# Kernel tuning notes

Measured on AMD Instinct MI355X. Metric: run time of the kernel, lower is better.

Reference implementation:

```python
import jax, jax.numpy as jnp
import numpy as np

DIM = 192
HEADS = 6
HEAD_DIM = DIM // HEADS
SCALE = HEAD_DIM ** -0.5
WIN = (2, 6, 12)  # (pl, lat, lon)
RES = (8, 96, 360)
TOW = (RES[0] // WIN[0]) * (RES[1] // WIN[1])  # type_of_windows = 64
N = WIN[0] * WIN[1] * WIN[2]  # 144
NW = TOW
B_ = 1 * (RES[2] // WIN[2])  # 30
TABLE = WIN[0] ** 2 * WIN[1] ** 2 * (2 * WIN[2] - 1)  # 3312


def get_earth_position_index(ws):
    wpl, wlat, wlon = ws
    czi = np.arange(wpl)
    czj = -np.arange(wpl) * wpl
    chi = np.arange(wlat)
    chj = -np.arange(wlat) * wlat
    cw = np.arange(wlon)
    c1 = np.stack(np.meshgrid(czi, chi, cw, indexing='ij'))
    c2 = np.stack(np.meshgrid(czj, chj, cw, indexing='ij'))
    f1 = c1.reshape(3, -1)
    f2 = c2.reshape(3, -1)
    coords = (f1[:, :, None] - f2[:, None, :]).transpose(1, 2, 0).copy()
    coords[:, :, 2] += wlon - 1
    coords[:, :, 1] *= 2 * wlon - 1
    coords[:, :, 0] *= (2 * wlon - 1) * wlat * wlat
    return coords.sum(-1)  # [N, N]


def setup_inputs() -> dict:
    key = jax.random.key(0)
    ks = jax.random.split(key, 6)
    x = jax.random.normal(ks[0], (B_, NW, N, DIM), dtype=jnp.float32)
    qkv_w = jax.random.normal(ks[1], (3 * DIM, DIM), dtype=jnp.float32) * 0.02
    qkv_b = jnp.zeros((3 * DIM,), dtype=jnp.float32)
    proj_w = jax.random.normal(ks[2], (DIM, DIM), dtype=jnp.float32) * 0.02
    proj_b = jnp.zeros((DIM,), dtype=jnp.float32)
    bias_table = jax.random.normal(ks[3], (TABLE, TOW, HEADS), dtype=jnp.float32) * 0.02
    pos_index = jnp.asarray(get_earth_position_index(WIN), dtype=jnp.int32)
    return {"x": x, "qkv_w": qkv_w, "qkv_b": qkv_b, "proj_w": proj_w,
            "proj_b": proj_b, "bias_table": bias_table, "pos_index": pos_index}


def reference(x, qkv_w, qkv_b, proj_w, proj_b, bias_table, pos_index):
    Bw, nW, n, C = x.shape
    # fused qkv projection
    qkv = jnp.einsum('bwnc,dc->bwnd', x, qkv_w) + qkv_b
    qkv = qkv.reshape(Bw, nW, n, 3, HEADS, HEAD_DIM)
    q = qkv[..., 0, :, :].transpose(0, 3, 1, 2, 4) * SCALE  # [B,H,W,N,hd]
    k = qkv[..., 1, :, :].transpose(0, 3, 1, 2, 4)
    v = qkv[..., 2, :, :].transpose(0, 3, 1, 2, 4)
    attn = jnp.einsum('bhwnd,bhwmd->bhwnm', q, k)  # [B,H,W,N,N]
    # gathered earth position bias: [N,N,TOW,H] -> [H,TOW,N,N]
    bias = bias_table[pos_index.reshape(-1)].reshape(n, n, TOW, HEADS)
    bias = bias.transpose(3, 2, 0, 1)
    attn = attn + bias[None]
    attn = jax.nn.softmax(attn, axis=-1)
    out = jnp.einsum('bhwnm,bhwmd->bhwnd', attn, v)
    out = out.transpose(0, 2, 3, 1, 4).reshape(Bw, nW, n, C)
    out = jnp.einsum('bwnc,dc->bwnd', out, proj_w) + proj_b
    return out
```

## Files before the change

kernel.cpp:

```cpp
#include <hip/hip_runtime.h>

typedef unsigned short u16;
typedef unsigned int u32;

#define NTOK 144
#define CDIM 192
#define NHEADS 6
#define HDIM 32
#define NWIN 64
#define NB 30
#define NBLK (NB * NWIN)
#define TABLE_N 3312
#define SCALE 0.17677669529663687f

typedef __bf16 bf16x8 __attribute__((ext_vector_type(8)));
typedef u16 u16x8 __attribute__((ext_vector_type(8)));
typedef u16 u16x4 __attribute__((ext_vector_type(4)));
typedef float f32x4 __attribute__((ext_vector_type(4)));

__device__ __forceinline__ float bf2f(u16 u) {
    union { u32 i; float f; } v; v.i = ((u32)u) << 16; return v.f;
}
__device__ __forceinline__ u16 f2bf(float f) {
    union { float f; u32 i; } v; v.f = f;
    u32 r = v.i + 0x7FFFu + ((v.i >> 16) & 1u);
    return (u16)(r >> 16);
}

__device__ __forceinline__ bf16x8 ld_frag(const void* base, size_t idx, int fm) {
    if (!fm) return *(const bf16x8*)((const u16*)base + idx);
    const float* pf = (const float*)base;
    u16x8 t;
#pragma unroll
    for (int j = 0; j < 8; ++j) t[j] = f2bf(pf[idx + j]);
    union { u16x8 u; bf16x8 b; } cv; cv.u = t; return cv.b;
}
__device__ __forceinline__ float ld_s(const void* base, size_t idx, int fm) {
    return fm ? ((const float*)base)[idx] : bf2f(((const u16*)base)[idx]);
}
__device__ __forceinline__ void st_s(void* base, size_t idx, float v, int fm) {
    if (fm) ((float*)base)[idx] = v; else ((u16*)base)[idx] = f2bf(v);
}
__device__ __forceinline__ bf16x8 zero_frag() {
    union { u16x8 u; bf16x8 b; } cv;
#pragma unroll
    for (int j = 0; j < 8; ++j) cv.u[j] = 0;
    return cv.b;
}
__device__ __forceinline__ bf16x8 ld_x_frag(const void* x, size_t rowbase, int off, int fm) {
    if (!fm) return *(const bf16x8*)((const u16*)x + rowbase + off);
    const float* xs = (const float*)x + rowbase + off;
    const float4 a0 = *(const float4*)xs;
    const float4 a1 = *(const float4*)(xs + 4);
    union { u16x8 u; bf16x8 b; } cv;
    cv.u[0] = f2bf(a0.x); cv.u[1] = f2bf(a0.y); cv.u[2] = f2bf(a0.z); cv.u[3] = f2bf(a0.w);
    cv.u[4] = f2bf(a1.x); cv.u[5] = f2bf(a1.y); cv.u[6] = f2bf(a1.z); cv.u[7] = f2bf(a1.w);
    return cv.b;
}

__global__ void detect_mode(const u16* __restrict__ w, int* __restrict__ flag) {
    __shared__ int cnt;
    if (threadIdx.x == 0) cnt = 0;
    __syncthreads();
    int h = 0;
    for (int i = threadIdx.x; i < 4096; i += 256) {
        int e = (w[i] >> 7) & 0xFF;
        if (e >= 0x8E) h++;
    }
    atomicAdd(&cnt, h);
    __syncthreads();
    if (threadIdx.x == 0) flag[0] = (cnt > 64) ? 1 : 0;
}

__global__ void bias_gather3(const void* __restrict__ table, const int* __restrict__ pos,
                             u16* __restrict__ bias_f, const int* __restrict__ mode) {
    __shared__ u16 smT[TABLE_N];
    const int fm = mode[0];
    const int w = blockIdx.x / NHEADS, h = blockIdx.x % NHEADS;
    for (int t = threadIdx.x; t < TABLE_N; t += 256) {
        size_t j = (size_t)t * (NWIN * NHEADS) + w * NHEADS + h;
        smT[t] = fm ? f2bf(((const float*)table)[j]) : ((const u16*)table)[j];
    }
    __syncthreads();
    u16* o = bias_f + (size_t)(w * NHEADS + h) * (81 * 256);
    for (int i = threadIdx.x; i < 81 * 256; i += 256) {
        int T = i / 2304, rem2 = i % 2304;
        int nt = rem2 >> 8, lane = (rem2 >> 2) & 63, r = rem2 & 3;
        int row = T * 16 + (lane >> 4) * 4 + r;
        int col = nt * 16 + (lane & 15);
        o[i] = smT[pos[row * NTOK + col]];
    }
}

__global__ void wconv(const void* __restrict__ qkv_w, const void* __restrict__ qkv_b,
                      const void* __restrict__ proj_w, const void* __restrict__ proj_b,
                      u16* __restrict__ qkvw_c, u16* __restrict__ projw_c,
                      u16* __restrict__ qkvb_c, u16* __restrict__ projb_c,
                      const int* __restrict__ mode) {
    const int fm = mode[0];
    const int gid = blockIdx.x * blockDim.x + threadIdx.x;
    const int np  = gridDim.x * blockDim.x;
    const int NQW = 3 * CDIM * CDIM, NPW = CDIM * CDIM;
    if (fm) {
        const float* a = (const float*)qkv_w;
        const float* b = (const float*)proj_w;
        const float* c = (const float*)qkv_b;
        const float* d = (const float*)proj_b;
        for (int i = gid; i < NQW; i += np) qkvw_c[i] = f2bf(a[i]);
        for (int i = gid; i < NPW; i += np) projw_c[i] = f2bf(b[i]);
        for (int i = gid; i < 3 * CDIM; i += np) qkvb_c[i] = f2bf(c[i]);
        for (int i = gid; i < CDIM; i += np) projb_c[i] = f2bf(d[i]);
    } else {
        const u16* a = (const u16*)qkv_w;
        const u16* b = (const u16*)proj_w;
        const u16* c = (const u16*)qkv_b;
        const u16* d = (const u16*)proj_b;
        for (int i = gid; i < NQW; i += np) qkvw_c[i] = a[i];
        for (int i = gid; i < NPW; i += np) projw_c[i] = b[i];
        for (int i = gid; i < 3 * CDIM; i += np) qkvb_c[i] = c[i];
        for (int i = gid; i < CDIM; i += np) projb_c[i] = d[i];
    }
}

#define AQ_OFF  0
#define AK_OFF  5760
#define AQK_STR 40
#define APB_OFF 11520
#define AP_STR  152
#define AW_STR  200
#define AVT_OFF 33408
#define AVT_STR 152
#define ASM_TOT 38272

__global__ __launch_bounds__(576, 8)
void attn_qkv(const void* __restrict__ x,
              const u16* __restrict__ qkvw_c, const u16* __restrict__ qkvb_c,
              const u16* __restrict__ bias_f, u16* __restrict__ o_ws,
              const int* __restrict__ mode) {
    __shared__ __align__(16) u16 sm[ASM_TOT];

    const int fm   = mode[0];
    const int tid  = threadIdx.x;
    const int wv   = tid >> 6;
    const int lane = tid & 63;
    const int l15  = lane & 15;
    const int lq   = lane >> 4;

    const int blk   = blockIdx.x;
    const int virt  = (blk & 7) * (NBLK / 8) + (blk >> 3);
    const int w     = virt / NB;
    const int bwlin = (virt % NB) * NWIN + w;

    const size_t xrow = ((size_t)bwlin * NTOK + wv * 16 + l15) * CDIM;
    const f32x4 fzero = {0.f, 0.f, 0.f, 0.f};

    for (int h = 0; h < NHEADS; ++h) {
        const int hoff = h * HDIM;

        for (int i = tid; i < 96 * CDIM / 8; i += 576) {
            int r = i / 24, c8 = (i % 24) * 8;
            int grow = (r >> 5) * CDIM + hoff + (r & 31);
            *(uint4*)&sm[APB_OFF + r * AW_STR + c8] =
                *(const uint4*)(qkvw_c + (size_t)grow * CDIM + c8);
        }
        __syncthreads();

        {
            f32x4 acc[6];
#pragma unroll
            for (int nt = 0; nt < 6; ++nt) acc[nt] = fzero;
#pragma unroll
            for (int kt = 0; kt < 6; ++kt) {
                bf16x8 xf = ld_x_frag(x, xrow, kt * 32 + lq * 8, fm);
#pragma unroll
                for (int nt = 0; nt < 6; ++nt) {
                    bf16x8 bb = *(const bf16x8*)&sm[APB_OFF + (nt * 16 + l15) * AW_STR + kt * 32 + lq * 8];
                    acc[nt] = __builtin_amdgcn_mfma_f32_16x16x32_bf16(xf, bb, acc[nt], 0, 0, 0);
                }
            }
#pragma unroll
            for (int nt = 0; nt < 6; ++nt) {
                int col = nt * 16 + l15;
                int s = col >> 5, d = col & 31;
                float bias = bf2f(qkvb_c[s * CDIM + hoff + d]);
#pragma unroll
                for (int r = 0; r < 4; ++r) {
                    int row = wv * 16 + lq * 4 + r;
                    float v = acc[nt][r] + bias;
                    if (s == 0)      sm[AQ_OFF + row * AQK_STR + d] = f2bf(v * SCALE);
                    else if (s == 1) sm[AK_OFF + row * AQK_STR + d] = f2bf(v);
                    else             sm[AVT_OFF + d * AVT_STR + row] = f2bf(v);
                }
            }
        }
        __syncthreads();

        f32x4 sacc[9];
        {
            bf16x8 a = *(const bf16x8*)&sm[AQ_OFF + (wv * 16 + l15) * AQK_STR + lq * 8];
#pragma unroll
            for (int nt = 0; nt < 9; ++nt) {
                bf16x8 bb = *(const bf16x8*)&sm[AK_OFF + (nt * 16 + l15) * AQK_STR + lq * 8];
                sacc[nt] = __builtin_amdgcn_mfma_f32_16x16x32_bf16(a, bb, fzero, 0, 0, 0);
            }
            const u16* bf = bias_f + ((size_t)(w * NHEADS + h) * 81 + wv * 9) * 256;
#pragma unroll
            for (int nt = 0; nt < 9; ++nt) {
                u16x4 pk = *(const u16x4*)&bf[nt * 256 + (lane << 2)];
#pragma unroll
                for (int r = 0; r < 4; ++r) sacc[nt][r] += bf2f(pk[r]);
            }
#pragma unroll
            for (int r = 0; r < 4; ++r) {
                float m = -1e30f;
                for (int nt = 0; nt < 9; ++nt) m = fmaxf(m, sacc[nt][r]);
                for (int d = 1; d < 16; d <<= 1) m = fmaxf(m, __shfl_xor(m, d, 64));
                float s = 0.f;
                for (int nt = 0; nt < 9; ++nt) {
                    float e = __expf(sacc[nt][r] - m);
                    sacc[nt][r] = e; s += e;
                }
                for (int d = 1; d < 16; d <<= 1) s += __shfl_xor(s, d, 64);
                float inv = 1.0f / s;
                for (int nt = 0; nt < 9; ++nt) sacc[nt][r] *= inv;
            }
        }

#pragma unroll
        for (int r = 0; r < 4; ++r) {
            int row = wv * 16 + lq * 4 + r;
#pragma unroll
            for (int nt = 0; nt < 9; ++nt)
                sm[APB_OFF + row * AP_STR + nt * 16 + l15] = f2bf(sacc[nt][r]);
        }
        __syncthreads();

        {
            f32x4 pv[2] = {fzero, fzero};
#pragma unroll
            for (int kt = 0; kt < 4; ++kt) {
                bf16x8 a = *(const bf16x8*)&sm[APB_OFF + (wv * 16 + l15) * AP_STR + kt * 32 + lq * 8];
#pragma unroll
                for (int dt = 0; dt < 2; ++dt) {
                    bf16x8 bb = *(const bf16x8*)&sm[AVT_OFF + (dt * 16 + l15) * AVT_STR + kt * 32 + lq * 8];
                    pv[dt] = __builtin_amdgcn_mfma_f32_16x16x32_bf16(a, bb, pv[dt], 0, 0, 0);
                }
            }
            bf16x8 a4 = zero_frag();
            if (lq < 2)
                a4 = *(const bf16x8*)&sm[APB_OFF + (wv * 16 + l15) * AP_STR + 128 + lq * 8];
#pragma unroll
            for (int dt = 0; dt < 2; ++dt) {
                bf16x8 bb = *(const bf16x8*)&sm[AVT_OFF + (dt * 16 + l15) * AVT_STR + 128 + (lq & 1) * 8];
                pv[dt] = __builtin_amdgcn_mfma_f32_16x16x32_bf16(a4, bb, pv[dt], 0, 0, 0);
            }
            u16* op = o_ws + (((size_t)h * NBLK + bwlin) * NTOK + wv * 16 + lq * 4) * HDIM;
#pragma unroll
            for (int dt = 0; dt < 2; ++dt)
#pragma unroll
                for (int r = 0; r < 4; ++r)
                    op[r * HDIM + dt * 16 + l15] = f2bf(pv[dt][r]);
        }
        __syncthreads();
    }
}

#define PW_STR 200
__global__ __launch_bounds__(512, 4)
void proj_gemm(const u16* __restrict__ o_ws, const u16* __restrict__ projw_c,
               const u16* __restrict__ projb_c, void* __restrict__ out,
               const int* __restrict__ mode) {
    __shared__ __align__(16) u16 smW[CDIM * PW_STR];
    const int fm   = mode[0];
    const int tid  = threadIdx.x;
    const int wv   = tid >> 6;
    const int lane = tid & 63;
    const int l15  = lane & 15;
    const int lq   = lane >> 4;

    for (int i = tid; i < CDIM * CDIM / 8; i += 512) {
        int r = i / 24, c8 = (i % 24) * 8;
        *(uint4*)&smW[r * PW_STR + c8] = *(const uint4*)(projw_c + (size_t)r * CDIM + c8);
    }
    __syncthreads();

    const int tile = blockIdx.x * 8 + wv;
    const int win  = tile / 9;
    const int trow = (tile % 9) * 16;
    const f32x4 fzero = {0.f, 0.f, 0.f, 0.f};

    bf16x8 a[6];
#pragma unroll
    for (int kt = 0; kt < 6; ++kt)
        a[kt] = *(const bf16x8*)&o_ws[((size_t)kt * NBLK + win) * (NTOK * HDIM)
                                      + (trow + l15) * HDIM + lq * 8];

    f32x4 acc[12];
#pragma unroll
    for (int nt = 0; nt < 12; ++nt) acc[nt] = fzero;
#pragma unroll
    for (int kt = 0; kt < 6; ++kt) {
#pragma unroll
        for (int nt = 0; nt < 12; ++nt) {
            bf16x8 bb = *(const bf16x8*)&smW[(nt * 16 + l15) * PW_STR + kt * 32 + lq * 8];
            acc[nt] = __builtin_amdgcn_mfma_f32_16x16x32_bf16(a[kt], bb, acc[nt], 0, 0, 0);
        }
    }
    const size_t rb = (size_t)win * (NTOK * CDIM) + (size_t)trow * CDIM;
#pragma unroll
    for (int nt = 0; nt < 12; ++nt) {
        int col = nt * 16 + l15;
        float pb = bf2f(projb_c[col]);
#pragma unroll
        for (int r = 0; r < 4; ++r)
            st_s(out, rb + (lq * 4 + r) * CDIM + col, acc[nt][r] + pb, fm);
    }
}

#define Q_OFF  0
#define K_OFF  5760
#define QK_STR 40
#define P_OFF  11520
#define P_STR  168
#define VT_OFF 35712
#define VT_STR 168
#define OA_OFF 41088
#define OA_STR 200
#define SM_TOT 69888

template<int FASTW>
__global__ __launch_bounds__(576, 3)
void earth_attn_fused(const void* __restrict__ x, const void* __restrict__ qkv_w,
                const void* __restrict__ qkv_b, const void* __restrict__ proj_w,
                const void* __restrict__ proj_b, const void* __restrict__ bias_table,
                const int* __restrict__ pos_index,
                const u16* __restrict__ qkvw_c, const u16* __restrict__ projw_c,
                const u16* __restrict__ qkvb_c, const u16* __restrict__ projb_c,
                const u16* __restrict__ bias_f, int use_bias_f,
                void* __restrict__ out, const int* __restrict__ mode) {
    __shared__ __align__(16) u16 sm[SM_TOT];

    const int fm   = mode[0];
    const int tid  = threadIdx.x;
    const int wv   = tid >> 6;
    const int lane = tid & 63;
    const int l15  = lane & 15;
    const int lq   = lane >> 4;

    const int blk   = blockIdx.x;
    const int virt  = (blk & 7) * (NBLK / 8) + (blk >> 3);
    const int w     = virt / NB;
    const int bwlin = (virt % NB) * NWIN + w;

    {
        uint4 z; z.x = z.y = z.z = z.w = 0u;
        for (int i = tid; i < (32 * VT_STR) / 8; i += 576) *(uint4*)&sm[VT_OFF + i * 8] = z;
    }

    bf16x8 xfrag[6];
    {
        const size_t xrow = ((size_t)bwlin * NTOK + wv * 16 + l15) * CDIM;
#pragma unroll
        for (int kt = 0; kt < 6; ++kt) xfrag[kt] = ld_x_frag(x, xrow, kt * 32 + lq * 8, fm);
    }
    __syncthreads();

    const f32x4 fzero = {0.f, 0.f, 0.f, 0.f};

    for (int h = 0; h < NHEADS; ++h) {
        const int hoff = h * HDIM;

        float bsv[9][4];
        if (FASTW || use_bias_f) {
            const u16* bf = bias_f + ((size_t)(w * NHEADS + h) * 81 + wv * 9) * 256;
#pragma unroll
            for (int nt = 0; nt < 9; ++nt) {
                u16x4 pk = *(const u16x4*)&bf[nt * 256 + (lane << 2)];
#pragma unroll
                for (int r = 0; r < 4; ++r) bsv[nt][r] = bf2f(pk[r]);
            }
        } else {
#pragma unroll
            for (int nt = 0; nt < 9; ++nt) {
                int col = nt * 16 + l15;
#pragma unroll
                for (int r = 0; r < 4; ++r) {
                    int idx = pos_index[(wv * 16 + lq * 4 + r) * NTOK + col];
                    bsv[nt][r] = ld_s(bias_table, ((size_t)idx * NWIN + w) * NHEADS + h, fm);
                }
            }
        }

        {
            f32x4 acc[6];
            for (int nt = 0; nt < 6; ++nt) acc[nt] = fzero;
            int wrow[6];
#pragma unroll
            for (int nt = 0; nt < 6; ++nt) {
                int c = nt * 16 + l15, s = c >> 5, d = c & 31;
                wrow[nt] = (s * CDIM + hoff + d) * CDIM;
            }
#pragma unroll
            for (int kt = 0; kt < 6; ++kt) {
#pragma unroll
                for (int nt = 0; nt < 6; ++nt) {
                    bf16x8 bb = FASTW
                        ? *(const bf16x8*)&qkvw_c[(size_t)wrow[nt] + kt * 32 + lq * 8]
                        : ld_frag(qkv_w, (size_t)wrow[nt] + kt * 32 + lq * 8, fm);
                    acc[nt] = __builtin_amdgcn_mfma_f32_16x16x32_bf16(xfrag[kt], bb, acc[nt], 0, 0, 0);
                }
            }
#pragma unroll
            for (int nt = 0; nt < 6; ++nt) {
                int col = nt * 16 + l15;
                int s = col >> 5, d = col & 31;
                float bias = FASTW ? bf2f(qkvb_c[s * CDIM + hoff + d])
                                   : ld_s(qkv_b, s * CDIM + hoff + d, fm);
#pragma unroll
                for (int r = 0; r < 4; ++r) {
                    int row = wv * 16 + lq * 4 + r;
                    float v = acc[nt][r] + bias;
                    if (s == 0)      sm[Q_OFF + row * QK_STR + d] = f2bf(v * SCALE);
                    else if (s == 1) sm[K_OFF + row * QK_STR + d] = f2bf(v);
                    else             sm[VT_OFF + d * VT_STR + row] = f2bf(v);
                }
            }
        }
        __syncthreads();

        f32x4 sacc[9];
        {
            bf16x8 a = *(const bf16x8*)&sm[Q_OFF + (wv * 16 + l15) * QK_STR + lq * 8];
#pragma unroll
            for (int nt = 0; nt < 9; ++nt) {
                bf16x8 bb = *(const bf16x8*)&sm[K_OFF + (nt * 16 + l15) * QK_STR + lq * 8];
                sacc[nt] = __builtin_amdgcn_mfma_f32_16x16x32_bf16(a, bb, fzero, 0, 0, 0);
            }
#pragma unroll
            for (int nt = 0; nt < 9; ++nt)
#pragma unroll
                for (int r = 0; r < 4; ++r) sacc[nt][r] += bsv[nt][r];
#pragma unroll
            for (int r = 0; r < 4; ++r) {
                float m = -1e30f;
                for (int nt = 0; nt < 9; ++nt) m = fmaxf(m, sacc[nt][r]);
                for (int d = 1; d < 16; d <<= 1) m = fmaxf(m, __shfl_xor(m, d, 64));
                float s = 0.f;
                for (int nt = 0; nt < 9; ++nt) {
                    float e = __expf(sacc[nt][r] - m);
                    sacc[nt][r] = e; s += e;
                }
                for (int d = 1; d < 16; d <<= 1) s += __shfl_xor(s, d, 64);
                float inv = 1.0f / s;
                for (int nt = 0; nt < 9; ++nt) sacc[nt][r] *= inv;
            }
        }

#pragma unroll
        for (int r = 0; r < 4; ++r) {
            int row = wv * 16 + lq * 4 + r;
#pragma unroll
            for (int nt = 0; nt < 9; ++nt)
                sm[P_OFF + row * P_STR + nt * 16 + l15] = f2bf(sacc[nt][r]);
            sm[P_OFF + row * P_STR + 144 + l15] = 0;
        }
        __syncthreads();

        f32x4 pv[2] = {fzero, fzero};
#pragma unroll
        for (int kt = 0; kt < 5; ++kt) {
            bf16x8 a = *(const bf16x8*)&sm[P_OFF + (wv * 16 + l15) * P_STR + kt * 32 + lq * 8];
#pragma unroll
            for (int dt = 0; dt < 2; ++dt) {
                bf16x8 bb = *(const bf16x8*)&sm[VT_OFF + (dt * 16 + l15) * VT_STR + kt * 32 + lq * 8];
                pv[dt] = __builtin_amdgcn_mfma_f32_16x16x32_bf16(a, bb, pv[dt], 0, 0, 0);
            }
        }

#pragma unroll
        for (int dt = 0; dt < 2; ++dt)
#pragma unroll
            for (int r = 0; r < 4; ++r) {
                int row = wv * 16 + lq * 4 + r;
                sm[OA_OFF + row * OA_STR + hoff + dt * 16 + l15] = f2bf(pv[dt][r]);
            }
        __syncthreads();
    }

    f32x4 oacc[12];
    for (int nt = 0; nt < 12; ++nt) oacc[nt] = fzero;
    {
        bf16x8 a[6];
#pragma unroll
        for (int kt = 0; kt < 6; ++kt)
            a[kt] = *(const bf16x8*)&sm[OA_OFF + (wv * 16 + l15) * OA_STR + kt * 32 + lq * 8];
#pragma unroll
        for (int kt = 0; kt < 6; ++kt) {
#pragma unroll
            for (int nt = 0; nt < 12; ++nt) {
                bf16x8 bb = FASTW
                    ? *(const bf16x8*)&projw_c[(size_t)(nt * 16 + l15) * CDIM + kt * 32 + lq * 8]
                    : ld_frag(proj_w, (size_t)(nt * 16 + l15) * CDIM + kt * 32 + lq * 8, fm);
                oacc[nt] = __builtin_amdgcn_mfma_f32_16x16x32_bf16(a[kt], bb, oacc[nt], 0, 0, 0);
            }
        }
    }

    const size_t obase = (size_t)bwlin * (NTOK * CDIM);
#pragma unroll
    for (int nt = 0; nt < 12; ++nt) {
        int col = nt * 16 + l15;
        float pb = FASTW ? bf2f(projb_c[col]) : ld_s(proj_b, col, fm);
#pragma unroll
        for (int r = 0; r < 4; ++r) {
            int row = wv * 16 + lq * 4 + r;
            st_s(out, obase + row * CDIM + col, oacc[nt][r] + pb, fm);
        }
    }
}

extern "C" void kernel_launch(void* const* d_in, const int* in_sizes, int n_in,
                              void* d_out, int out_size, void* d_ws, size_t ws_size,
                              hipStream_t stream) {
    const void* x          = d_in[0];
    const void* qkv_w      = d_in[1];
    const void* qkv_b      = d_in[2];
    const void* proj_w     = d_in[3];
    const void* proj_b     = d_in[4];
    const void* bias_table = d_in[5];
    const int*  pos_index  = (const int*)d_in[6];

    int*  mode_flag = (int*)d_ws;
    char* p         = (char*)d_ws + 16;
    const size_t biasf_bytes = (size_t)NWIN * NHEADS * 81 * 256 * sizeof(u16);
    u16* bias_f = (u16*)p;            p += biasf_bytes;
    u16* qkvw_c = (u16*)p;            p += (size_t)3 * CDIM * CDIM * sizeof(u16);
    u16* projw_c = (u16*)p;           p += (size_t)CDIM * CDIM * sizeof(u16);
    u16* qkvb_c = (u16*)p;            p += 3 * CDIM * sizeof(u16);
    u16* projb_c = (u16*)p;           p += CDIM * sizeof(u16);
    const size_t need_w = (size_t)(p - (char*)d_ws);
    u16* o_ws = (u16*)p;              p += (size_t)NHEADS * NBLK * NTOK * HDIM * sizeof(u16);
    const size_t need_split = (size_t)(p - (char*)d_ws);
    const size_t need_biasf = 16 + biasf_bytes;

    int use_bias_f = (ws_size >= need_biasf) ? 1 : 0;
    int use_w      = (ws_size >= need_w) ? 1 : 0;
    int use_split  = (ws_size >= need_split) ? 1 : 0;

    detect_mode<<<dim3(1), dim3(256), 0, stream>>>((const u16*)qkv_w, mode_flag);
    if (use_bias_f)
        bias_gather3<<<dim3(NWIN * NHEADS), dim3(256), 0, stream>>>(
            bias_table, pos_index, bias_f, mode_flag);
    if (use_w)
        wconv<<<dim3(192), dim3(256), 0, stream>>>(
            qkv_w, qkv_b, proj_w, proj_b, qkvw_c, projw_c, qkvb_c, projb_c, mode_flag);

    if (use_split) {
        attn_qkv<<<dim3(NBLK), dim3(576), 0, stream>>>(
            x, qkvw_c, qkvb_c, bias_f, o_ws, mode_flag);
        proj_gemm<<<dim3(NBLK * 9 / 8), dim3(512), 0, stream>>>(
            o_ws, projw_c, projb_c, d_out, mode_flag);
    } else if (use_w) {
        earth_attn_fused<1><<<dim3(NBLK), dim3(576), 0, stream>>>(
            x, qkv_w, qkv_b, proj_w, proj_b, bias_table, pos_index,
            qkvw_c, projw_c, qkvb_c, projb_c, bias_f, 1, d_out, mode_flag);
    } else {
        earth_attn_fused<0><<<dim3(NBLK), dim3(576), 0, stream>>>(
            x, qkv_w, qkv_b, proj_w, proj_b, bias_table, pos_index,
            qkvw_c, projw_c, qkvb_c, projb_c, bias_f, use_bias_f, d_out, mode_flag);
    }
}
```

Baseline: 851.3 us.

## Split fused QKV+attention into separate QKV GEMM and per-head attention kernels

```diff
diff --git a/kernel.cpp b/kernel.cpp
--- a/kernel.cpp
+++ b/kernel.cpp
@@ -122,22 +122,13 @@
     }
 }
 
-#define AQ_OFF  0
-#define AK_OFF  5760
-#define AQK_STR 40
-#define APB_OFF 11520
-#define AP_STR  152
-#define AW_STR  200
-#define AVT_OFF 33408
-#define AVT_STR 152
-#define ASM_TOT 38272
-
-__global__ __launch_bounds__(576, 8)
-void attn_qkv(const void* __restrict__ x,
+#define GW_STR 200
+__global__ __launch_bounds__(512, 8)
+void qkv_gemm(const void* __restrict__ x,
               const u16* __restrict__ qkvw_c, const u16* __restrict__ qkvb_c,
-              const u16* __restrict__ bias_f, u16* __restrict__ o_ws,
+              u16* __restrict__ q_ws, u16* __restrict__ k_ws, u16* __restrict__ v_ws,
               const int* __restrict__ mode) {
-    __shared__ __align__(16) u16 sm[ASM_TOT];
+    __shared__ __align__(16) u16 smW[96 * GW_STR];
 
     const int fm   = mode[0];
     const int tid  = threadIdx.x;
@@ -151,21 +142,21 @@
     const int w     = virt / NB;
     const int bwlin = (virt % NB) * NWIN + w;
 
-    const size_t xrow = ((size_t)bwlin * NTOK + wv * 16 + l15) * CDIM;
     const f32x4 fzero = {0.f, 0.f, 0.f, 0.f};
 
     for (int h = 0; h < NHEADS; ++h) {
         const int hoff = h * HDIM;
 
-        for (int i = tid; i < 96 * CDIM / 8; i += 576) {
+        for (int i = tid; i < 96 * CDIM / 8; i += 512) {
             int r = i / 24, c8 = (i % 24) * 8;
             int grow = (r >> 5) * CDIM + hoff + (r & 31);
-            *(uint4*)&sm[APB_OFF + r * AW_STR + c8] =
-                *(const uint4*)(qkvw_c + (size_t)grow * CDIM + c8);
-        }
-        __syncthreads();
-
-        {
+            *(uint4*)&smW[r * GW_STR + c8] = *(const uint4*)(qkvw_c + (size_t)grow * CDIM + c8);
+        }
+        __syncthreads();
+
+        const size_t obase = ((size_t)bwlin * NHEADS + h) * (NTOK * HDIM);
+        for (int t = wv; t < 9; t += 8) {
+            const size_t xrow = ((size_t)bwlin * NTOK + t * 16 + l15) * CDIM;
             f32x4 acc[6];
 #pragma unroll
             for (int nt = 0; nt < 6; ++nt) acc[nt] = fzero;
@@ -174,7 +165,7 @@
                 bf16x8 xf = ld_x_frag(x, xrow, kt * 32 + lq * 8, fm);
 #pragma unroll
                 for (int nt = 0; nt < 6; ++nt) {
-                    bf16x8 bb = *(const bf16x8*)&sm[APB_OFF + (nt * 16 + l15) * AW_STR + kt * 32 + lq * 8];
+                    bf16x8 bb = *(const bf16x8*)&smW[(nt * 16 + l15) * GW_STR + kt * 32 + lq * 8];
                     acc[nt] = __builtin_amdgcn_mfma_f32_16x16x32_bf16(xf, bb, acc[nt], 0, 0, 0);
                 }
             }
@@ -185,83 +176,128 @@
                 float bias = bf2f(qkvb_c[s * CDIM + hoff + d]);
 #pragma unroll
                 for (int r = 0; r < 4; ++r) {
-                    int row = wv * 16 + lq * 4 + r;
+                    int row = t * 16 + lq * 4 + r;
                     float v = acc[nt][r] + bias;
-                    if (s == 0)      sm[AQ_OFF + row * AQK_STR + d] = f2bf(v * SCALE);
-                    else if (s == 1) sm[AK_OFF + row * AQK_STR + d] = f2bf(v);
-                    else             sm[AVT_OFF + d * AVT_STR + row] = f2bf(v);
-                }
-            }
-        }
-        __syncthreads();
-
+                    size_t idx = obase + (size_t)row * HDIM + d;
+                    if (s == 0)      q_ws[idx] = f2bf(v * SCALE);
+                    else if (s == 1) k_ws[idx] = f2bf(v);
+                    else             v_ws[idx] = f2bf(v);
+                }
+            }
+        }
+        __syncthreads();
+    }
+}
+
+#define BK_OFF  0
+#define BK_STR  40
+#define BVT_OFF 5760
+#define BVT_STR 152
+#define BP_OFF  10624
+#define BP_TILE 2432
+#define BSM_TOT 32512
+
+__global__ __launch_bounds__(512, 4)
+void attn_bh(const u16* __restrict__ q_ws, const u16* __restrict__ k_ws,
+             const u16* __restrict__ v_ws, const u16* __restrict__ bias_f,
+             u16* __restrict__ o_ws) {
+    __shared__ __align__(16) u16 sm[BSM_TOT];
+
+    const int tid  = threadIdx.x;
+    const int wv   = tid >> 6;
+    const int lane = tid & 63;
+    const int l15  = lane & 15;
+    const int lq   = lane >> 4;
+
+    const int blk  = blockIdx.x;
+    const int virt = (blk & 7) * (NBLK * NHEADS / 8) + (blk >> 3);
+    const int w    = virt / (NB * NHEADS);
+    const int rem  = virt % (NB * NHEADS);
+    const int h    = rem / NB;
+    const int b    = rem % NB;
+    const int bwlin = b * NWIN + w;
+
+    const size_t kvbase = ((size_t)bwlin * NHEADS + h) * (NTOK * HDIM);
+
+    for (int i = tid; i < 576; i += 512) {
+        int r = i >> 2, c8 = (i & 3) * 8;
+        *(uint4*)&sm[BK_OFF + r * BK_STR + c8] = *(const uint4*)(k_ws + kvbase + (size_t)r * HDIM + c8);
+    }
+    for (int i = tid; i < 576; i += 512) {
+        int m = i >> 2, c8 = (i & 3) * 8;
+        u16x8 vv = *(const u16x8*)(v_ws + kvbase + (size_t)m * HDIM + c8);
+#pragma unroll
+        for (int j = 0; j < 8; ++j)
+            sm[BVT_OFF + (c8 + j) * BVT_STR + m] = vv[j];
+    }
+    __syncthreads();
+
+    const f32x4 fzero = {0.f, 0.f, 0.f, 0.f};
+
+    for (int t = wv; t < 9; t += 8) {
         f32x4 sacc[9];
         {
-            bf16x8 a = *(const bf16x8*)&sm[AQ_OFF + (wv * 16 + l15) * AQK_STR + lq * 8];
+            bf16x8 a = *(const bf16x8*)(q_ws + kvbase + (size_t)(t * 16 + l15) * HDIM + lq * 8);
 #pragma unroll
             for (int nt = 0; nt < 9; ++nt) {
-                bf16x8 bb = *(const bf16x8*)&sm[AK_OFF + (nt * 16 + l15) * AQK_STR + lq * 8];
+                bf16x8 bb = *(const bf16x8*)&sm[BK_OFF + (nt * 16 + l15) * BK_STR + lq * 8];
                 sacc[nt] = __builtin_amdgcn_mfma_f32_16x16x32_bf16(a, bb, fzero, 0, 0, 0);
             }
-            const u16* bf = bias_f + ((size_t)(w * NHEADS + h) * 81 + wv * 9) * 256;
+        }
+        {
+            const u16* bf = bias_f + ((size_t)(w * NHEADS + h) * 81 + t * 9) * 256;
 #pragma unroll
             for (int nt = 0; nt < 9; ++nt) {
                 u16x4 pk = *(const u16x4*)&bf[nt * 256 + (lane << 2)];
 #pragma unroll
                 for (int r = 0; r < 4; ++r) sacc[nt][r] += bf2f(pk[r]);
             }
-#pragma unroll
-            for (int r = 0; r < 4; ++r) {
-                float m = -1e30f;
-                for (int nt = 0; nt < 9; ++nt) m = fmaxf(m, sacc[nt][r]);
-                for (int d = 1; d < 16; d <<= 1) m = fmaxf(m, __shfl_xor(m, d, 64));
-                float s = 0.f;
-                for (int nt = 0; nt < 9; ++nt) {
-                    float e = __expf(sacc[nt][r] - m);
-                    sacc[nt][r] = e; s += e;
-                }
-                for (int d = 1; d < 16; d <<= 1) s += __shfl_xor(s, d, 64);
-                float inv = 1.0f / s;
-                for (int nt = 0; nt < 9; ++nt) sacc[nt][r] *= inv;
-            }
-        }
-
+        }
 #pragma unroll
         for (int r = 0; r < 4; ++r) {
-            int row = wv * 16 + lq * 4 + r;
+            float m = -1e30f;
+            for (int nt = 0; nt < 9; ++nt) m = fmaxf(m, sacc[nt][r]);
+            for (int d = 1; d < 16; d <<= 1) m = fmaxf(m, __shfl_xor(m, d, 64));
+            float s = 0.f;
+            for (int nt = 0; nt < 9; ++nt) {
+                float e = __expf(sacc[nt][r] - m);
+                sacc[nt][r] = e; s += e;
+            }
+            for (int d = 1; d < 16; d <<= 1) s += __shfl_xor(s, d, 64);
+            float inv = 1.0f / s;
+            for (int nt = 0; nt < 9; ++nt) sacc[nt][r] *= inv;
+        }
+        u16* pt = &sm[BP_OFF + t * BP_TILE];
+#pragma unroll
+        for (int r = 0; r < 4; ++r) {
+            int row = lq * 4 + r;
 #pragma unroll
             for (int nt = 0; nt < 9; ++nt)
-                sm[APB_OFF + row * AP_STR + nt * 16 + l15] = f2bf(sacc[nt][r]);
-        }
-        __syncthreads();
-
-        {
-            f32x4 pv[2] = {fzero, fzero};
-#pragma unroll
-            for (int kt = 0; kt < 4; ++kt) {
-                bf16x8 a = *(const bf16x8*)&sm[APB_OFF + (wv * 16 + l15) * AP_STR + kt * 32 + lq * 8];
-#pragma unroll
-                for (int dt = 0; dt < 2; ++dt) {
-                    bf16x8 bb = *(const bf16x8*)&sm[AVT_OFF + (dt * 16 + l15) * AVT_STR + kt * 32 + lq * 8];
-                    pv[dt] = __builtin_amdgcn_mfma_f32_16x16x32_bf16(a, bb, pv[dt], 0, 0, 0);
-                }
-            }
-            bf16x8 a4 = zero_frag();
-            if (lq < 2)
-                a4 = *(const bf16x8*)&sm[APB_OFF + (wv * 16 + l15) * AP_STR + 128 + lq * 8];
+                pt[row * BVT_STR + nt * 16 + l15] = f2bf(sacc[nt][r]);
+        }
+        f32x4 pv[2] = {fzero, fzero};
+#pragma unroll
+        for (int kt = 0; kt < 4; ++kt) {
+            bf16x8 a = *(const bf16x8*)&pt[l15 * BVT_STR + kt * 32 + lq * 8];
 #pragma unroll
             for (int dt = 0; dt < 2; ++dt) {
-                bf16x8 bb = *(const bf16x8*)&sm[AVT_OFF + (dt * 16 + l15) * AVT_STR + 128 + (lq & 1) * 8];
-                pv[dt] = __builtin_amdgcn_mfma_f32_16x16x32_bf16(a4, bb, pv[dt], 0, 0, 0);
-            }
-            u16* op = o_ws + (((size_t)h * NBLK + bwlin) * NTOK + wv * 16 + lq * 4) * HDIM;
-#pragma unroll
-            for (int dt = 0; dt < 2; ++dt)
-#pragma unroll
-                for (int r = 0; r < 4; ++r)
-                    op[r * HDIM + dt * 16 + l15] = f2bf(pv[dt][r]);
-        }
-        __syncthreads();
+                bf16x8 bb = *(const bf16x8*)&sm[BVT_OFF + (dt * 16 + l15) * BVT_STR + kt * 32 + lq * 8];
+                pv[dt] = __builtin_amdgcn_mfma_f32_16x16x32_bf16(a, bb, pv[dt], 0, 0, 0);
+            }
+        }
+        bf16x8 a4 = zero_frag();
+        if (lq < 2) a4 = *(const bf16x8*)&pt[l15 * BVT_STR + 128 + lq * 8];
+#pragma unroll
+        for (int dt = 0; dt < 2; ++dt) {
+            bf16x8 bb = *(const bf16x8*)&sm[BVT_OFF + (dt * 16 + l15) * BVT_STR + 128 + (lq & 1) * 8];
+            pv[dt] = __builtin_amdgcn_mfma_f32_16x16x32_bf16(a4, bb, pv[dt], 0, 0, 0);
+        }
+        u16* op = o_ws + (((size_t)h * NBLK + bwlin) * NTOK + t * 16 + lq * 4) * HDIM;
+#pragma unroll
+        for (int dt = 0; dt < 2; ++dt)
+#pragma unroll
+            for (int r = 0; r < 4; ++r)
+                op[r * HDIM + dt * 16 + l15] = f2bf(pv[dt][r]);
     }
 }
 
@@ -317,6 +353,149 @@
     }
 }
 
+#define AQ_OFF  0
+#define AK_OFF  5760
+#define AQK_STR 40
+#define APB_OFF 11520
+#define AP_STR  152
+#define AW_STR  200
+#define AVT_OFF 33408
+#define AVT_STR 152
+#define ASM_TOT 38272
+
+__global__ __launch_bounds__(576, 8)
+void attn_qkv(const void* __restrict__ x,
+              const u16* __restrict__ qkvw_c, const u16* __restrict__ qkvb_c,
+              const u16* __restrict__ bias_f, u16* __restrict__ o_ws,
+              const int* __restrict__ mode) {
+    __shared__ __align__(16) u16 sm[ASM_TOT];
+
+    const int fm   = mode[0];
+    const int tid  = threadIdx.x;
+    const int wv   = tid >> 6;
+    const int lane = tid & 63;
+    const int l15  = lane & 15;
+    const int lq   = lane >> 4;
+
+    const int blk   = blockIdx.x;
+    const int virt  = (blk & 7) * (NBLK / 8) + (blk >> 3);
+    const int w     = virt / NB;
+    const int bwlin = (virt % NB) * NWIN + w;
+
+    const size_t xrow = ((size_t)bwlin * NTOK + wv * 16 + l15) * CDIM;
+    const f32x4 fzero = {0.f, 0.f, 0.f, 0.f};
+
+    for (int h = 0; h < NHEADS; ++h) {
+        const int hoff = h * HDIM;
+
+        for (int i = tid; i < 96 * CDIM / 8; i += 576) {
+            int r = i / 24, c8 = (i % 24) * 8;
+            int grow = (r >> 5) * CDIM + hoff + (r & 31);
+            *(uint4*)&sm[APB_OFF + r * AW_STR + c8] =
+                *(const uint4*)(qkvw_c + (size_t)grow * CDIM + c8);
+        }
+        __syncthreads();
+
+        {
+            f32x4 acc[6];
+#pragma unroll
+            for (int nt = 0; nt < 6; ++nt) acc[nt] = fzero;
+#pragma unroll
+            for (int kt = 0; kt < 6; ++kt) {
+                bf16x8 xf = ld_x_frag(x, xrow, kt * 32 + lq * 8, fm);
+#pragma unroll
+                for (int nt = 0; nt < 6; ++nt) {
+                    bf16x8 bb = *(const bf16x8*)&sm[APB_OFF + (nt * 16 + l15) * AW_STR + kt * 32 + lq * 8];
+                    acc[nt] = __builtin_amdgcn_mfma_f32_16x16x32_bf16(xf, bb, acc[nt], 0, 0, 0);
+                }
+            }
+#pragma unroll
+            for (int nt = 0; nt < 6; ++nt) {
+                int col = nt * 16 + l15;
+                int s = col >> 5, d = col & 31;
+                float bias = bf2f(qkvb_c[s * CDIM + hoff + d]);
+#pragma unroll
+                for (int r = 0; r < 4; ++r) {
+                    int row = wv * 16 + lq * 4 + r;
+                    float v = acc[nt][r] + bias;
+                    if (s == 0)      sm[AQ_OFF + row * AQK_STR + d] = f2bf(v * SCALE);
+                    else if (s == 1) sm[AK_OFF + row * AQK_STR + d] = f2bf(v);
+                    else             sm[AVT_OFF + d * AVT_STR + row] = f2bf(v);
+                }
+            }
+        }
+        __syncthreads();
+
+        f32x4 sacc[9];
+        {
+            bf16x8 a = *(const bf16x8*)&sm[AQ_OFF + (wv * 16 + l15) * AQK_STR + lq * 8];
+#pragma unroll
+            for (int nt = 0; nt < 9; ++nt) {
+                bf16x8 bb = *(const bf16x8*)&sm[AK_OFF + (nt * 16 + l15) * AQK_STR + lq * 8];
+                sacc[nt] = __builtin_amdgcn_mfma_f32_16x16x32_bf16(a, bb, fzero, 0, 0, 0);
+            }
+            const u16* bf = bias_f + ((size_t)(w * NHEADS + h) * 81 + wv * 9) * 256;
+#pragma unroll
+            for (int nt = 0; nt < 9; ++nt) {
+                u16x4 pk = *(const u16x4*)&bf[nt * 256 + (lane << 2)];
+#pragma unroll
+                for (int r = 0; r < 4; ++r) sacc[nt][r] += bf2f(pk[r]);
+            }
+#pragma unroll
+            for (int r = 0; r < 4; ++r) {
+                float m = -1e30f;
+                for (int nt = 0; nt < 9; ++nt) m = fmaxf(m, sacc[nt][r]);
+                for (int d = 1; d < 16; d <<= 1) m = fmaxf(m, __shfl_xor(m, d, 64));
+                float s = 0.f;
+                for (int nt = 0; nt < 9; ++nt) {
+                    float e = __expf(sacc[nt][r] - m);
+                    sacc[nt][r] = e; s += e;
+                }
+                for (int d = 1; d < 16; d <<= 1) s += __shfl_xor(s, d, 64);
+                float inv = 1.0f / s;
+                for (int nt = 0; nt < 9; ++nt) sacc[nt][r] *= inv;
+            }
+        }
+
+#pragma unroll
+        for (int r = 0; r < 4; ++r) {
+            int row = wv * 16 + lq * 4 + r;
+#pragma unroll
+            for (int nt = 0; nt < 9; ++nt)
+                sm[APB_OFF + row * AP_STR + nt * 16 + l15] = f2bf(sacc[nt][r]);
+        }
+        __syncthreads();
+
+        {
+            f32x4 pv[2] = {fzero, fzero};
+#pragma unroll
+            for (int kt = 0; kt < 4; ++kt) {
+                bf16x8 a = *(const bf16x8*)&sm[APB_OFF + (wv * 16 + l15) * AP_STR + kt * 32 + lq * 8];
+#pragma unroll
+                for (int dt = 0; dt < 2; ++dt) {
+                    bf16x8 bb = *(const bf16x8*)&sm[AVT_OFF + (dt * 16 + l15) * AVT_STR + kt * 32 + lq * 8];
+                    pv[dt] = __builtin_amdgcn_mfma_f32_16x16x32_bf16(a, bb, pv[dt], 0, 0, 0);
+                }
+            }
+            bf16x8 a4 = zero_frag();
+            if (lq < 2)
+                a4 = *(const bf16x8*)&sm[APB_OFF + (wv * 16 + l15) * AP_STR + 128 + lq * 8];
+#pragma unroll
+            for (int dt = 0; dt < 2; ++dt) {
+                bf16x8 bb = *(const bf16x8*)&sm[AVT_OFF + (dt * 16 + l15) * AVT_STR + 128 + (lq & 1) * 8];
+                pv[dt] = __builtin_amdgcn_mfma_f32_16x16x32_bf16(a4, bb, pv[dt], 0, 0, 0);
+            }
+            u16* op = o_ws + (((size_t)h * NBLK + bwlin) * NTOK + wv * 16 + lq * 4) * HDIM;
+#pragma unroll
+            for (int dt = 0; dt < 2; ++dt)
+#pragma unroll
+                for (int r = 0; r < 4; ++r)
+                    op[r * HDIM + dt * 16 + l15] = f2bf(pv[dt][r]);
+        }
+        __syncthreads();
+    }
+}
+
 #define Q_OFF  0
 #define K_OFF  5760
 #define QK_STR 40
@@ -328,15 +507,11 @@
 #define OA_STR 200
 #define SM_TOT 69888
 
-template<int FASTW>
 __global__ __launch_bounds__(576, 3)
 void earth_attn_fused(const void* __restrict__ x, const void* __restrict__ qkv_w,
                 const void* __restrict__ qkv_b, const void* __restrict__ proj_w,
                 const void* __restrict__ proj_b, const void* __restrict__ bias_table,
                 const int* __restrict__ pos_index,
-                const u16* __restrict__ qkvw_c, const u16* __restrict__ projw_c,
-                const u16* __restrict__ qkvb_c, const u16* __restrict__ projb_c,
-                const u16* __restrict__ bias_f, int use_bias_f,
                 void* __restrict__ out, const int* __restrict__ mode) {
     __shared__ __align__(16) u16 sm[SM_TOT];
 
@@ -371,23 +546,13 @@
         const int hoff = h * HDIM;
 
         float bsv[9][4];
-        if (FASTW || use_bias_f) {
-            const u16* bf = bias_f + ((size_t)(w * NHEADS + h) * 81 + wv * 9) * 256;
-#pragma unroll
-            for (int nt = 0; nt < 9; ++nt) {
-                u16x4 pk = *(const u16x4*)&bf[nt * 256 + (lane << 2)];
-#pragma unroll
-                for (int r = 0; r < 4; ++r) bsv[nt][r] = bf2f(pk[r]);
-            }
-        } else {
-#pragma unroll
-            for (int nt = 0; nt < 9; ++nt) {
-                int col = nt * 16 + l15;
-#pragma unroll
-                for (int r = 0; r < 4; ++r) {
-                    int idx = pos_index[(wv * 16 + lq * 4 + r) * NTOK + col];
-                    bsv[nt][r] = ld_s(bias_table, ((size_t)idx * NWIN + w) * NHEADS + h, fm);
-                }
+#pragma unroll
+        for (int nt = 0; nt < 9; ++nt) {
+            int col = nt * 16 + l15;
+#pragma unroll
+            for (int r = 0; r < 4; ++r) {
+                int idx = pos_index[(wv * 16 + lq * 4 + r) * NTOK + col];
+                bsv[nt][r] = ld_s(bias_table, ((size_t)idx * NWIN + w) * NHEADS + h, fm);
             }
         }
 
@@ -404,9 +569,7 @@
             for (int kt = 0; kt < 6; ++kt) {
 #pragma unroll
                 for (int nt = 0; nt < 6; ++nt) {
-                    bf16x8 bb = FASTW
-                        ? *(const bf16x8*)&qkvw_c[(size_t)wrow[nt] + kt * 32 + lq * 8]
-                        : ld_frag(qkv_w, (size_t)wrow[nt] + kt * 32 + lq * 8, fm);
+                    bf16x8 bb = ld_frag(qkv_w, (size_t)wrow[nt] + kt * 32 + lq * 8, fm);
                     acc[nt] = __builtin_amdgcn_mfma_f32_16x16x32_bf16(xfrag[kt], bb, acc[nt], 0, 0, 0);
                 }
             }
@@ -414,8 +577,7 @@
             for (int nt = 0; nt < 6; ++nt) {
                 int col = nt * 16 + l15;
                 int s = col >> 5, d = col & 31;
-                float bias = FASTW ? bf2f(qkvb_c[s * CDIM + hoff + d])
-                                   : ld_s(qkv_b, s * CDIM + hoff + d, fm);
+                float bias = ld_s(qkv_b, s * CDIM + hoff + d, fm);
 #pragma unroll
                 for (int r = 0; r < 4; ++r) {
                     int row = wv * 16 + lq * 4 + r;
@@ -498,9 +660,7 @@
         for (int kt = 0; kt < 6; ++kt) {
 #pragma unroll
             for (int nt = 0; nt < 12; ++nt) {
-                bf16x8 bb = FASTW
-                    ? *(const bf16x8*)&projw_c[(size_t)(nt * 16 + l15) * CDIM + kt * 32 + lq * 8]
-                    : ld_frag(proj_w, (size_t)(nt * 16 + l15) * CDIM + kt * 32 + lq * 8, fm);
+                bf16x8 bb = ld_frag(proj_w, (size_t)(nt * 16 + l15) * CDIM + kt * 32 + lq * 8, fm);
                 oacc[nt] = __builtin_amdgcn_mfma_f32_16x16x32_bf16(a[kt], bb, oacc[nt], 0, 0, 0);
             }
         }
@@ -510,7 +670,7 @@
 #pragma unroll
     for (int nt = 0; nt < 12; ++nt) {
         int col = nt * 16 + l15;
-        float pb = FASTW ? bf2f(projb_c[col]) : ld_s(proj_b, col, fm);
+        float pb = ld_s(proj_b, col, fm);
 #pragma unroll
         for (int r = 0; r < 4; ++r) {
             int row = wv * 16 + lq * 4 + r;
@@ -538,35 +698,40 @@
     u16* projw_c = (u16*)p;           p += (size_t)CDIM * CDIM * sizeof(u16);
     u16* qkvb_c = (u16*)p;            p += 3 * CDIM * sizeof(u16);
     u16* projb_c = (u16*)p;           p += CDIM * sizeof(u16);
-    const size_t need_w = (size_t)(p - (char*)d_ws);
-    u16* o_ws = (u16*)p;              p += (size_t)NHEADS * NBLK * NTOK * HDIM * sizeof(u16);
-    const size_t need_split = (size_t)(p - (char*)d_ws);
-    const size_t need_biasf = 16 + biasf_bytes;
-
-    int use_bias_f = (ws_size >= need_biasf) ? 1 : 0;
-    int use_w      = (ws_size >= need_w) ? 1 : 0;
-    int use_split  = (ws_size >= need_split) ? 1 : 0;
+    const size_t plane = (size_t)NBLK * NHEADS * NTOK * HDIM * sizeof(u16);
+    u16* o_ws = (u16*)p;              p += plane;
+    const size_t need_split2 = (size_t)(p - (char*)d_ws);
+    u16* q_ws = (u16*)p;              p += plane;
+    u16* k_ws = (u16*)p;              p += plane;
+    u16* v_ws = (u16*)p;              p += plane;
+    const size_t need_split3 = (size_t)(p - (char*)d_ws);
+
+    int use_split2 = (ws_size >= need_split2) ? 1 : 0;
+    int use_split3 = (ws_size >= need_split3) ? 1 : 0;
 
     detect_mode<<<dim3(1), dim3(256), 0, stream>>>((const u16*)qkv_w, mode_flag);
-    if (use_bias_f)
+
+    if (use_split2) {
         bias_gather3<<<dim3(NWIN * NHEADS), dim3(256), 0, stream>>>(
             bias_table, pos_index, bias_f, mode_flag);
-    if (use_w)
         wconv<<<dim3(192), dim3(256), 0, stream>>>(
             qkv_w, qkv_b, proj_w, proj_b, qkvw_c, projw_c, qkvb_c, projb_c, mode_flag);
-
-    if (use_split) {
+    }
+
+    if (use_split3) {
+        qkv_gemm<<<dim3(NBLK), dim3(512), 0, stream>>>(
+            x, qkvw_c, qkvb_c, q_ws, k_ws, v_ws, mode_flag);
+        attn_bh<<<dim3(NBLK * NHEADS), dim3(512), 0, stream>>>(
+            q_ws, k_ws, v_ws, bias_f, o_ws);
+        proj_gemm<<<dim3(NBLK * 9 / 8), dim3(512), 0, stream>>>(
+            o_ws, projw_c, projb_c, d_out, mode_flag);
+    } else if (use_split2) {
         attn_qkv<<<dim3(NBLK), dim3(576), 0, stream>>>(
             x, qkvw_c, qkvb_c, bias_f, o_ws, mode_flag);
         proj_gemm<<<dim3(NBLK * 9 / 8), dim3(512), 0, stream>>>(
             o_ws, projw_c, projb_c, d_out, mode_flag);
-    } else if (use_w) {
-        earth_attn_fused<1><<<dim3(NBLK), dim3(576), 0, stream>>>(
-            x, qkv_w, qkv_b, proj_w, proj_b, bias_table, pos_index,
-            qkvw_c, projw_c, qkvb_c, projb_c, bias_f, 1, d_out, mode_flag);
     } else {
-        earth_attn_fused<0><<<dim3(NBLK), dim3(576), 0, stream>>>(
-            x, qkv_w, qkv_b, proj_w, proj_b, bias_table, pos_index,
-            qkvw_c, projw_c, qkvb_c, projb_c, bias_f, use_bias_f, d_out, mode_flag);
-    }
-}
+        earth_attn_fused<<<dim3(NBLK), dim3(576), 0, stream>>>(
+            x, qkv_w, qkv_b, proj_w, proj_b, bias_table, pos_index, d_out, mode_flag);
+    }
+}
```

Measured after the change: 2.381 ms. 180% more time.
